# Kernel optimization log

Measured on AMD Instinct MI355X. Metric: run time of the kernel, lower is better.

## Reference

```python
import jax, jax.numpy as jnp
import numpy as np

B, S, E, H = 8, 2048, 1024, 64  # batch, seq (== block_size), emb_size, head_size


def setup_inputs() -> dict:
    key = jax.random.key(0)
    ks = jax.random.split(key, 7)
    s = 1.0 / np.sqrt(E)  # ~ torch Linear default init scale
    return {
        "x": jax.random.normal(ks[0], (B, S, E), dtype=jnp.float32),
        "Wk": jax.random.uniform(ks[1], (H, E), jnp.float32, -s, s),
        "bk": jax.random.uniform(ks[2], (H,), jnp.float32, -s, s),
        "Wq": jax.random.uniform(ks[3], (H, E), jnp.float32, -s, s),
        "bq": jax.random.uniform(ks[4], (H,), jnp.float32, -s, s),
        "Wv": jax.random.uniform(ks[5], (H, E), jnp.float32, -s, s),
        "bv": jax.random.uniform(ks[6], (H,), jnp.float32, -s, s),
    }


def reference(x, Wk, bk, Wq, bq, Wv, bv):
    # Linear projections (torch Linear: y = x @ W.T + b)
    xk = jnp.einsum('bse,he->bsh', x, Wk) + bk  # [B,S,H]
    xq = jnp.einsum('bse,he->bsh', x, Wq) + bq
    xv = jnp.einsum('bse,he->bsh', x, Wv) + bv
    # raw scores q @ k^T  -> [B,S,S]
    wei = jnp.einsum('bqh,bkh->bqk', xq, xk)
    # causal mask (encoder=True branch in source; tril==0 -> -inf)
    causal = jnp.tril(jnp.ones((x.shape[1], x.shape[1]), dtype=bool))
    wei = jnp.where(causal, wei, -jnp.inf)
    # NOTE: source divides by head_size**(-0.5), i.e. MULTIPLIES by sqrt(head_size)
    scale = jnp.asarray(Wk.shape[0], jnp.float32) ** 0.5
    wei = jax.nn.softmax(wei * scale, axis=-1)
    return jnp.einsum('bqk,bkh->bqh', wei, xv)
```

## Files before the change

kernel.cpp:

```cpp
#include <hip/hip_runtime.h>

typedef _Float16 f16;
typedef _Float16 f16x8 __attribute__((ext_vector_type(8)));
typedef _Float16 f16x4 __attribute__((ext_vector_type(4)));
typedef __fp16 fp16x2 __attribute__((ext_vector_type(2)));
typedef float f32x4 __attribute__((ext_vector_type(4)));

#define MFMA16(a, b, c) __builtin_amdgcn_mfma_f32_16x16x32_f16(a, b, c, 0, 0, 0)

constexpr int Bn = 8, Sn = 2048, En = 1024, Hn = 64;
constexpr int Mn = Bn * Sn;
constexpr float QSCALE = 11.5415603f;
constexpr float THR = 11.5f;

__device__ __forceinline__ void gload_lds16(const void* g, void* lds) {
    __builtin_amdgcn_global_load_lds(
        (const __attribute__((address_space(1))) void*)g,
        (__attribute__((address_space(3))) void*)lds, 16, 0, 0);
}
__device__ __forceinline__ void wait_vm4() {
    asm volatile("s_waitcnt vmcnt(4)" ::: "memory");
    __builtin_amdgcn_sched_barrier(0);
}
__device__ __forceinline__ void wait_vm0() {
    asm volatile("s_waitcnt vmcnt(0)" ::: "memory");
    __builtin_amdgcn_sched_barrier(0);
}
__device__ __forceinline__ void barrier_raw() {
    __builtin_amdgcn_s_barrier();
    __builtin_amdgcn_sched_barrier(0);
}
__device__ __forceinline__ f16x8 cvt8(float4 lo, float4 hi) {
    union { f16x8 v; fp16x2 h[4]; } u;
    u.h[0] = __builtin_amdgcn_cvt_pkrtz(lo.x, lo.y);
    u.h[1] = __builtin_amdgcn_cvt_pkrtz(lo.z, lo.w);
    u.h[2] = __builtin_amdgcn_cvt_pkrtz(hi.x, hi.y);
    u.h[3] = __builtin_amdgcn_cvt_pkrtz(hi.z, hi.w);
    return u.v;
}

__global__ __launch_bounds__(256) void convw_kernel(
    const float* __restrict__ Wq, const float* __restrict__ Wk,
    const float* __restrict__ Wv, f16* __restrict__ Wc)
{
    const int h = blockIdx.x * 256 + threadIdx.x;
    const int kt = h / 1536;
    const int rem = h - kt * 1536;
    const int rr = rem >> 3;
    const int c = rem & 7;
    const int set = rr >> 6;
    const float* src = (set == 0 ? Wq : (set == 1 ? Wk : Wv))
                       + (size_t)(rr & 63) * En + kt * 64 + c * 8;
    float4 v0 = *reinterpret_cast<const float4*>(src);
    float4 v1 = *reinterpret_cast<const float4*>(src + 4);
    f16x8 o = cvt8(v0, v1);
    const int cs = c ^ (rr & 7);
    *reinterpret_cast<f16x8*>(Wc + (size_t)kt * 12288 + rr * 64 + cs * 8) = o;
}

__global__ __launch_bounds__(512) void proj_kernel(
    const float* __restrict__ x, const f16* __restrict__ Wc,
    const float* __restrict__ bq, const float* __restrict__ bk,
    const float* __restrict__ bv,
    f16* __restrict__ qws, f16* __restrict__ kws, f16* __restrict__ vtws)
{
    __shared__ __align__(16) char ldsb[2 * 32768];
    const int tid = threadIdx.x;
    const int w = tid >> 6, l = tid & 63;
    const int l15 = l & 15, lhi = l >> 4;
    const int rt = w & 1, nh = w >> 1;
    const int Mbase = blockIdx.x * 32;

    f32x4 acc[3];
#pragma unroll
    for (int i = 0; i < 3; ++i) acc[i] = (f32x4){0.f, 0.f, 0.f, 0.f};

    const int xr_s = w * 4 + (l >> 4);
    const int xc_s = (l & 15) ^ (xr_s & 7);

#define WSTAGE(buf, kb)                                                       \
    {                                                                         \
        const f16* wt_ = Wc + (size_t)(kb) * 12288;                           \
        _Pragma("unroll")                                                     \
        for (int r_ = 0; r_ < 3; ++r_)                                        \
            gload_lds16(wt_ + r_ * 4096 + w * 512 + l * 8,                    \
                        ldsb + (buf) * 32768 + r_ * 8192 + w * 1024);         \
    }

#define XSTAGE(buf, kb)                                                       \
    {                                                                         \
        const float* xs_ = x + (size_t)(Mbase + xr_s) * En + (kb) * 64        \
                           + xc_s * 4;                                        \
        gload_lds16(xs_, ldsb + (buf) * 32768 + 24576 + w * 1024);            \
    }

#define COMPUTE(buf)                                                          \
    {                                                                         \
        const int xrow_ = rt * 16 + l15;                                      \
        const char* xb_ = ldsb + (buf) * 32768 + 24576 + xrow_ * 256;         \
        f16x8 a_[2];                                                          \
        _Pragma("unroll")                                                     \
        for (int kc_ = 0; kc_ < 2; ++kc_) {                                   \
            const int c0_ = kc_ * 8 + lhi * 2;                                \
            float4 lo_ = *reinterpret_cast<const float4*>(                    \
                xb_ + ((c0_ ^ (l15 & 7)) * 16));                              \
            float4 hi_ = *reinterpret_cast<const float4*>(                    \
                xb_ + (((c0_ + 1) ^ (l15 & 7)) * 16));                        \
            a_[kc_] = cvt8(lo_, hi_);                                         \
        }                                                                     \
        _Pragma("unroll")                                                     \
        for (int i_ = 0; i_ < 3; ++i_) {                                      \
            const int row16_ = (nh * 3 + i_) * 16 + l15;                      \
            _Pragma("unroll")                                                 \
            for (int kc_ = 0; kc_ < 2; ++kc_) {                               \
                const int addr_ = (buf) * 32768 + row16_ * 128                \
                    + ((kc_ * 64 + lhi * 16) ^ ((l15 & 7) << 4));             \
                f16x8 b_ = *reinterpret_cast<const f16x8*>(ldsb + addr_);     \
                acc[i_] = MFMA16(a_[kc_], b_, acc[i_]);                       \
            }                                                                 \
        }                                                                     \
    }

    WSTAGE(0, 0);
    XSTAGE(0, 0);
#pragma unroll
    for (int i = 0; i < 16; ++i) {
        const int cur = i & 1;
        if (i < 15) {
            WSTAGE(cur ^ 1, i + 1);
            XSTAGE(cur ^ 1, i + 1);
            wait_vm4();
        } else {
            wait_vm0();
        }
        barrier_raw();
        COMPUTE(cur);
        barrier_raw();
    }
#undef WSTAGE
#undef XSTAGE
#undef COMPUTE

    const int batch = Mbase >> 11;
    const int r0 = Mbase + rt * 16 + lhi * 4;
#pragma unroll
    for (int i = 0; i < 3; ++i) {
        const int nt = nh * 3 + i;
        const int set = nt >> 2;
        const int h = (nt & 3) * 16 + l15;
        const float bias = (set == 0 ? bq : (set == 1 ? bk : bv))[h];
        if (set == 0) {
#pragma unroll
            for (int r = 0; r < 4; ++r)
                qws[(size_t)(r0 + r) * Hn + h] =
                    (f16)((acc[i][r] + bias) * QSCALE);
        } else if (set == 1) {
#pragma unroll
            for (int r = 0; r < 4; ++r)
                kws[(size_t)(r0 + r) * Hn + h] = (f16)(acc[i][r] + bias);
        } else {
            const int s0v = r0 & (Sn - 1);
            const int sp = (s0v & ~31) + ((s0v & 12) << 1)
                         + ((s0v & 16) ? 4 : 0);
            f16x4 hv = {(f16)(acc[i][0] + bias), (f16)(acc[i][1] + bias),
                        (f16)(acc[i][2] + bias), (f16)(acc[i][3] + bias)};
            *reinterpret_cast<f16x4*>(
                &vtws[(size_t)batch * Hn * Sn + (size_t)h * Sn + sp]) = hv;
        }
    }
}

__global__ __launch_bounds__(256, 3) void attn_kernel(
    const f16* __restrict__ qws, const f16* __restrict__ kws,
    const f16* __restrict__ vtws, float* __restrict__ out,
    float* __restrict__ slots)
{
    const int tid = threadIdx.x;
    const int w = tid >> 6, l = tid & 63;
    const int l15 = l & 15, lhi = l >> 4;

    const int L = blockIdx.x * 4 + w;
    const int u = (int)(((unsigned)L * 997u) % 2304u);
    const int b = u / 288;
    const int t = u - b * 288;
    int k = 0;
#pragma unroll
    for (int gg = 1; gg < 8; ++gg)
        if (t >= 4 * gg * (gg + 1)) k = gg;
    const int rem = t - 4 * k * (k + 1);
    const int jq = rem / (k + 1);
    const int c = rem - jq * (k + 1);
    const int J = 8 * k + jq;

    const int qbase = J * 32;
    const int nkt = J + 1;
    const int ts = c * 8;
    const int te = (ts + 8 < nkt) ? ts + 8 : nkt;
    const bool hasDiag = (te == nkt);
    const int nfull = te - (hasDiag ? 1 : 0);

    const f16* qb = qws + (size_t)b * Sn * Hn;
    const f16* kb = kws + (size_t)b * Sn * Hn;
    const f16* vtb = vtws + (size_t)b * Hn * Sn;

    f16x8 qf[2][2];
#pragma unroll
    for (int rs = 0; rs < 2; ++rs)
#pragma unroll
        for (int kc = 0; kc < 2; ++kc)
            qf[rs][kc] = *reinterpret_cast<const f16x8*>(
                &qb[(size_t)(qbase + rs * 16 + l15) * Hn + kc * 32 + lhi * 8]);

    f32x4 O[2][4];
#pragma unroll
    for (int rs = 0; rs < 2; ++rs)
#pragma unroll
        for (int nt = 0; nt < 4; ++nt) O[rs][nt] = (f32x4){0.f, 0.f, 0.f, 0.f};
    float m1[2] = {-1e30f, -1e30f}, l1[2] = {0.f, 0.f};

#define ATTN_ITER(KT, MASKED)                                                 \
    {                                                                         \
        const int kbase = (KT) * 32;                                          \
        f16x8 kf[2][2];                                                       \
        _Pragma("unroll") for (int nt = 0; nt < 2; ++nt)                      \
        _Pragma("unroll") for (int kc = 0; kc < 2; ++kc)                      \
            kf[nt][kc] = *reinterpret_cast<const f16x8*>(                     \
                &kb[(size_t)(kbase + nt * 16 + l15) * Hn + kc * 32            \
                    + lhi * 8]);                                              \
        f32x4 Sv[2][2];                                                       \
        _Pragma("unroll") for (int rs = 0; rs < 2; ++rs)                      \
        _Pragma("unroll") for (int nt = 0; nt < 2; ++nt) {                    \
            f32x4 sa = (f32x4){0.f, 0.f, 0.f, 0.f};                           \
            sa = MFMA16(kf[nt][0], qf[rs][0], sa);                            \
            sa = MFMA16(kf[nt][1], qf[rs][1], sa);                            \
            Sv[rs][nt] = sa;                                                  \
        }                                                                     \
        float tv[2][2][4];                                                    \
        float mx[2];                                                          \
        _Pragma("unroll") for (int rs = 0; rs < 2; ++rs) {                    \
            _Pragma("unroll") for (int nt = 0; nt < 2; ++nt)                  \
            _Pragma("unroll") for (int r = 0; r < 4; ++r) {                   \
                float v = Sv[rs][nt][r];                                      \
                if (MASKED) {                                                 \
                    const int key_ = nt * 16 + lhi * 4 + r;                   \
                    const int qq_ = rs * 16 + l15;                            \
                    v = (key_ <= qq_) ? v : -1e30f;                           \
                }                                                             \
                tv[rs][nt][r] = v;                                            \
            }                                                                 \
            float a0 = fmaxf(fmaxf(tv[rs][0][0], tv[rs][0][1]),               \
                             fmaxf(tv[rs][0][2], tv[rs][0][3]));              \
            float a1 = fmaxf(fmaxf(tv[rs][1][0], tv[rs][1][1]),               \
                             fmaxf(tv[rs][1][2], tv[rs][1][3]));              \
            float m_ = fmaxf(a0, a1);                                         \
            m_ = fmaxf(m_, __shfl_xor(m_, 16));                               \
            m_ = fmaxf(m_, __shfl_xor(m_, 32));                               \
            mx[rs] = m_;                                                      \
        }                                                                     \
        const int need = (mx[0] > m1[0] + THR) || (mx[1] > m1[1] + THR);      \
        if (__any(need)) {                                                    \
            _Pragma("unroll") for (int rs = 0; rs < 2; ++rs) {                \
                const float mn = fmaxf(m1[rs], mx[rs]);                       \
                const float al = exp2f(m1[rs] - mn);                          \
                l1[rs] *= al;                                                 \
                _Pragma("unroll") for (int nt = 0; nt < 4; ++nt)              \
                _Pragma("unroll") for (int r = 0; r < 4; ++r)                 \
                    O[rs][nt][r] *= al;                                       \
                m1[rs] = mn;                                                  \
            }                                                                 \
        }                                                                     \
        f16x8 pa[2];                                                          \
        _Pragma("unroll") for (int rs = 0; rs < 2; ++rs) {                    \
            float p_[8];                                                      \
            float s_ = 0.f;                                                   \
            _Pragma("unroll") for (int nt = 0; nt < 2; ++nt)                  \
            _Pragma("unroll") for (int r = 0; r < 4; ++r) {                   \
                const float e_ = exp2f(tv[rs][nt][r] - m1[rs]);               \
                p_[nt * 4 + r] = e_;                                          \
                s_ += e_;                                                     \
            }                                                                 \
            s_ += __shfl_xor(s_, 16);                                         \
            s_ += __shfl_xor(s_, 32);                                         \
            l1[rs] += s_;                                                     \
            pa[rs] = (f16x8){(f16)p_[0], (f16)p_[1], (f16)p_[2], (f16)p_[3],  \
                             (f16)p_[4], (f16)p_[5], (f16)p_[6], (f16)p_[7]}; \
        }                                                                     \
        _Pragma("unroll") for (int nt = 0; nt < 4; ++nt) {                    \
            f16x8 vf = *reinterpret_cast<const f16x8*>(                       \
                &vtb[(size_t)(nt * 16 + l15) * Sn + kbase + lhi * 8]);        \
            O[0][nt] = MFMA16(vf, pa[0], O[0][nt]);                           \
            O[1][nt] = MFMA16(vf, pa[1], O[1][nt]);                           \
        }                                                                     \
    }

    for (int kt = ts; kt < nfull; ++kt) ATTN_ITER(kt, false);
    if (hasDiag) ATTN_ITER(J, true);
#undef ATTN_ITER

    if (J < 8) {
#pragma unroll
        for (int rs = 0; rs < 2; ++rs) {
            const float inv = 1.0f / l1[rs];
            const size_t ro = ((size_t)b * Sn + qbase + rs * 16 + l15) * Hn;
#pragma unroll
            for (int nt = 0; nt < 4; ++nt) {
                float4 o = {O[rs][nt][0] * inv, O[rs][nt][1] * inv,
                            O[rs][nt][2] * inv, O[rs][nt][3] * inv};
                *reinterpret_cast<float4*>(&out[ro + nt * 16 + lhi * 4]) = o;
            }
        }
    } else {
        float* sl = slots + (size_t)(b * 280 + 4 * k * (k + 1) - 8
                                     + jq * (k + 1) + c) * 1088;
        f16* so = reinterpret_cast<f16*>(sl + 64);
#pragma unroll
        for (int rs = 0; rs < 2; ++rs) {
            const int row = rs * 16 + l15;
            const float inv = 1.0f / l1[rs];
            if (lhi == 0) { sl[row] = m1[rs]; sl[32 + row] = l1[rs]; }
#pragma unroll
            for (int nt = 0; nt < 4; ++nt) {
                f16x4 hv = {(f16)(O[rs][nt][0] * inv), (f16)(O[rs][nt][1] * inv),
                            (f16)(O[rs][nt][2] * inv), (f16)(O[rs][nt][3] * inv)};
                *reinterpret_cast<f16x4*>(
                    &so[row * 64 + nt * 16 + lhi * 4]) = hv;
            }
        }
    }
}

__global__ __launch_bounds__(256) void comb_kernel(
    const float* __restrict__ slots, float* __restrict__ out)
{
    const int id = blockIdx.x;
    const int b = id / 56, jj = id - b * 56;
    const int J = 8 + jj;
    const int k = J >> 3;
    const int nch = k + 1;
    const float* base = slots + (size_t)(b * 280 + 4 * k * (k + 1) - 8
                                         + (J - 8 * k) * (k + 1)) * 1088;
    const int tid = threadIdx.x;
    const int row = tid >> 3;
    const int h0 = (tid & 7) * 8;

    float mg = -1e30f;
    for (int cc = 0; cc < nch; ++cc)
        mg = fmaxf(mg, base[cc * 1088 + row]);
    float den = 0.f;
    float num[8] = {0.f, 0.f, 0.f, 0.f, 0.f, 0.f, 0.f, 0.f};
    for (int cc = 0; cc < nch; ++cc) {
        const float* sl = base + cc * 1088;
        const float wgt = sl[32 + row] * exp2f(sl[row] - mg);
        den += wgt;
        const f16* so = reinterpret_cast<const f16*>(sl + 64);
        f16x8 ov = *reinterpret_cast<const f16x8*>(&so[row * 64 + h0]);
#pragma unroll
        for (int i = 0; i < 8; ++i) num[i] += (float)ov[i] * wgt;
    }
    const float inv = 1.0f / den;
    const size_t ro = ((size_t)b * Sn + J * 32 + row) * Hn + h0;
    float4 o0 = {num[0] * inv, num[1] * inv, num[2] * inv, num[3] * inv};
    float4 o1 = {num[4] * inv, num[5] * inv, num[6] * inv, num[7] * inv};
    *reinterpret_cast<float4*>(&out[ro]) = o0;
    *reinterpret_cast<float4*>(&out[ro + 4]) = o1;
}

extern "C" void kernel_launch(void* const* d_in, const int* in_sizes, int n_in,
                              void* d_out, int out_size, void* d_ws, size_t ws_size,
                              hipStream_t stream) {
    const float* x  = (const float*)d_in[0];
    const float* Wk = (const float*)d_in[1];
    const float* bk = (const float*)d_in[2];
    const float* Wq = (const float*)d_in[3];
    const float* bq = (const float*)d_in[4];
    const float* Wv = (const float*)d_in[5];
    const float* bv = (const float*)d_in[6];

    f16* qws  = (f16*)d_ws;
    f16* kws  = qws + (size_t)Mn * Hn;
    f16* vtws = kws + (size_t)Mn * Hn;
    f16* Wc   = vtws + (size_t)Mn * Hn;
    float* slots = (float*)(Wc + 196608);

    convw_kernel<<<96, 256, 0, stream>>>(Wq, Wk, Wv, Wc);
    proj_kernel<<<512, 512, 0, stream>>>(x, Wc, bq, bk, bv, qws, kws, vtws);
    attn_kernel<<<576, 256, 0, stream>>>(qws, kws, vtws, (float*)d_out, slots);
    comb_kernel<<<448, 256, 0, stream>>>(slots, (float*)d_out);
}
```

Measured before the change: 61.04 us.

## Store Q/K/V workspaces in MFMA-fragment order for contiguous attention loads

The projection epilogue now writes Q, K and V^T into a tiled layout where each 16x32 MFMA operand fragment occupies 512 contiguous halves, indexed by lane. The attention kernel then loads every fragment with one fully coalesced 16-byte-per-lane read (l*8), replacing the strided row accesses. The cost is that the projection stores Q and K one scalar element at a time at scattered addresses, which makes its epilogue less coalesced.

After: 53.28 us, median of 3. 1.15x faster.

```diff
diff --git a/kernel.cpp b/kernel.cpp
--- a/kernel.cpp
+++ b/kernel.cpp
@@ -38,6 +38,7 @@
     u.h[3] = __builtin_amdgcn_cvt_pkrtz(hi.z, hi.w);
     return u.v;
 }
+
 
 __global__ __launch_bounds__(256) void convw_kernel(
     const float* __restrict__ Wq, const float* __restrict__ Wk,
@@ -149,23 +150,34 @@
         const int set = nt >> 2;
         const int h = (nt & 3) * 16 + l15;
         const float bias = (set == 0 ? bq : (set == 1 ? bk : bv))[h];
-        if (set == 0) {
-#pragma unroll
-            for (int r = 0; r < 4; ++r)
-                qws[(size_t)(r0 + r) * Hn + h] =
-                    (f16)((acc[i][r] + bias) * QSCALE);
-        } else if (set == 1) {
-#pragma unroll
-            for (int r = 0; r < 4; ++r)
-                kws[(size_t)(r0 + r) * Hn + h] = (f16)(acc[i][r] + bias);
+        if (set < 2) {
+            f16* dst = (set == 0) ? qws : kws;
+            const float scale = (set == 0) ? QSCALE : 1.0f;
+            const int kc = h >> 5;
+            const int lhk = (h >> 3) & 3;
+            const int j = h & 7;
+#pragma unroll
+            for (int r = 0; r < 4; ++r) {
+                const int s = (r0 + r) & (Sn - 1);
+                const int t16 = s >> 4;
+                const int l15k = s & 15;
+                dst[(size_t)((batch * 128 + t16) * 2 + kc) * 512
+                    + (lhk * 16 + l15k) * 8 + j] =
+                    (f16)((acc[i][r] + bias) * scale);
+            }
         } else {
             const int s0v = r0 & (Sn - 1);
-            const int sp = (s0v & ~31) + ((s0v & 12) << 1)
-                         + ((s0v & 16) ? 4 : 0);
+            const int kt = s0v >> 5;
+            const int spl = ((s0v & 12) << 1) + ((s0v & 16) ? 4 : 0);
+            const int lhv = spl >> 3;
+            const int j0 = spl & 7;
+            const int ntv = h >> 4;
+            const int l15v = h & 15;
             f16x4 hv = {(f16)(acc[i][0] + bias), (f16)(acc[i][1] + bias),
                         (f16)(acc[i][2] + bias), (f16)(acc[i][3] + bias)};
             *reinterpret_cast<f16x4*>(
-                &vtws[(size_t)batch * Hn * Sn + (size_t)h * Sn + sp]) = hv;
+                &vtws[(size_t)((batch * 64 + kt) * 4 + ntv) * 512
+                      + (lhv * 16 + l15v) * 8 + j0]) = hv;
         }
     }
 }
@@ -199,17 +211,13 @@
     const bool hasDiag = (te == nkt);
     const int nfull = te - (hasDiag ? 1 : 0);
 
-    const f16* qb = qws + (size_t)b * Sn * Hn;
-    const f16* kb = kws + (size_t)b * Sn * Hn;
-    const f16* vtb = vtws + (size_t)b * Hn * Sn;
-
     f16x8 qf[2][2];
 #pragma unroll
     for (int rs = 0; rs < 2; ++rs)
 #pragma unroll
         for (int kc = 0; kc < 2; ++kc)
             qf[rs][kc] = *reinterpret_cast<const f16x8*>(
-                &qb[(size_t)(qbase + rs * 16 + l15) * Hn + kc * 32 + lhi * 8]);
+                &qws[(size_t)((b * 128 + J * 2 + rs) * 2 + kc) * 512 + l * 8]);
 
     f32x4 O[2][4];
 #pragma unroll
@@ -220,13 +228,12 @@
 
 #define ATTN_ITER(KT, MASKED)                                                 \
     {                                                                         \
-        const int kbase = (KT) * 32;                                          \
         f16x8 kf[2][2];                                                       \
         _Pragma("unroll") for (int nt = 0; nt < 2; ++nt)                      \
         _Pragma("unroll") for (int kc = 0; kc < 2; ++kc)                      \
             kf[nt][kc] = *reinterpret_cast<const f16x8*>(                     \
-                &kb[(size_t)(kbase + nt * 16 + l15) * Hn + kc * 32            \
-                    + lhi * 8]);                                              \
+                &kws[(size_t)((b * 128 + (KT) * 2 + nt) * 2 + kc) * 512       \
+                     + l * 8]);                                               \
         f32x4 Sv[2][2];                                                       \
         _Pragma("unroll") for (int rs = 0; rs < 2; ++rs)                      \
         _Pragma("unroll") for (int nt = 0; nt < 2; ++nt) {                    \
@@ -287,7 +294,7 @@
         }                                                                     \
         _Pragma("unroll") for (int nt = 0; nt < 4; ++nt) {                    \
             f16x8 vf = *reinterpret_cast<const f16x8*>(                       \
-                &vtb[(size_t)(nt * 16 + l15) * Sn + kbase + lhi * 8]);        \
+                &vtws[(size_t)((b * 64 + (KT)) * 4 + nt) * 512 + l * 8]);     \
             O[0][nt] = MFMA16(vf, pa[0], O[0][nt]);                           \
             O[1][nt] = MFMA16(vf, pa[1], O[1][nt]);                           \
         }                                                                     \
```
